# Optimization experiments

Measured on AMD Instinct MI355X. Metric: run time of the kernel, lower is better.

The kernel has to match this reference:

```python
import jax, jax.numpy as jnp
import numpy as np

N, H, C, A, G, NG = 400000, 256, 128, 32, 512, 1024
BN_EPS = 1e-5


def setup_inputs() -> dict:
    key = jax.random.key(0)
    ks = jax.random.split(key, 14)
    s = lambda fan: 1.0 / np.sqrt(fan)
    return {
        "initial_node_states": jax.random.normal(ks[0], (N, H), jnp.float32),
        "final_node_states": jax.random.normal(ks[1], (N, H), jnp.float32),
        "aux_variables": jax.random.normal(ks[2], (NG, A), jnp.float32),
        "graph_nodes_list": jnp.sort(jax.random.randint(ks[3], (N,), 0, NG, jnp.int32)),
        "num_graphs": NG,
        "Wg": jax.random.normal(ks[4], (2 * H, C), jnp.float32) * s(2 * H),
        "bg": jnp.zeros((C,), jnp.float32),
        "Wt": jax.random.normal(ks[5], (H, C), jnp.float32) * s(H),
        "bt": jnp.zeros((C,), jnp.float32),
        "gamma": jnp.ones((C + A,), jnp.float32),
        "beta": jnp.zeros((C + A,), jnp.float32),
        "W1": jax.random.normal(ks[6], (C + A, G), jnp.float32) * s(C + A),
        "b1": jnp.zeros((G,), jnp.float32),
        "W2": jax.random.normal(ks[7], (G, C), jnp.float32) * s(G),
        "b2": jnp.zeros((C,), jnp.float32),
    }


def reference(initial_node_states, final_node_states, aux_variables,
              graph_nodes_list, num_graphs,
              Wg, bg, Wt, bt, gamma, beta, W1, b1, W2, b2):
    # Nodewise gated readout (dropout layers are identity in eval mode)
    gate_input = jnp.concatenate([initial_node_states, final_node_states], axis=-1)  # [N, 2H]
    gate = jax.nn.sigmoid(gate_input @ Wg + bg)                                      # [N, C]
    nodewise = gate * (final_node_states @ Wt + bt)                                  # [N, C]
    # Scatter-add into per-graph buckets (index_add_)
    graph_readout = jax.ops.segment_sum(nodewise, graph_nodes_list, num_segments=num_graphs)  # [NG, C]
    ext = jnp.concatenate([graph_readout, aux_variables], axis=1)                    # [NG, C+A]
    # BatchNorm1d (training-mode batch statistics, biased variance)
    mean = ext.mean(axis=0)
    var = ext.var(axis=0)
    norm = (ext - mean) / jnp.sqrt(var + BN_EPS) * gamma + beta
    # Small MLP head
    hidden = jax.nn.relu(norm @ W1 + b1)
    logits = hidden @ W2 + b2                                                        # [NG, C]
    return logits
```

## Files before the change

kernel.cpp:

```cpp
#include <hip/hip_runtime.h>
#include <hip/hip_bf16.h>

#define NNODES 400000
#define BM 64

typedef __attribute__((ext_vector_type(8))) short  short8;
typedef __attribute__((ext_vector_type(4))) float  floatx4;

typedef unsigned short u16;
typedef unsigned int   u32;

__device__ __forceinline__ short f2bf(float f) {
    u32 u = __builtin_bit_cast(u32, f);
    u += 0x7fffu + ((u >> 16) & 1u);
    return (short)(u >> 16);
}

__device__ __forceinline__ void async16(const void* g, void* l) {
    __builtin_amdgcn_global_load_lds(
        (const __attribute__((address_space(1))) u32*)g,
        (__attribute__((address_space(3))) u32*)l, 16, 0, 0);
}

__global__ __launch_bounds__(256) void k0_build(
    const float* __restrict__ Wg, const float* __restrict__ Wt,
    u16* __restrict__ Bp)
{
    int base = (blockIdx.x * 256 + threadIdx.x) * 4;
    #pragma unroll
    for (int e = 0; e < 4; e++) {
        int idx  = base + e;
        int j    = idx & 7;
        int col  = (idx >> 3) & 255;
        int quad = (idx >> 11) & 3;
        int kc   = idx >> 13;
        int k    = kc * 32 + quad * 8 + j;
        float v;
        if (col < 128)       v = Wg[k * 128 + col];
        else if (k >= 256)   v = Wt[(k - 256) * 128 + (col - 128)];
        else                 v = 0.0f;
        Bp[idx] = (u16)f2bf(v);
    }
}

__global__ __launch_bounds__(256) void k1_gemm(
    const float* __restrict__ initS, const float* __restrict__ finS,
    const int* __restrict__ gids, const u16* __restrict__ Bp,
    const float* __restrict__ bg, const float* __restrict__ bt,
    float* __restrict__ readout)
{
    __shared__ __align__(16) u16  Bl[4][256][8];
    __shared__ float nodew[BM][128];
    __shared__ int   gidL[BM];

    const int tid  = threadIdx.x;
    const int w    = tid >> 6;
    const int lane = tid & 63;
    const int quad = lane >> 4;
    const int l15  = lane & 15;
    const int nodeBase = blockIdx.x * BM;

    if (tid < BM) gidL[tid] = gids[nodeBase + tid];

    floatx4 acc[16];
    #pragma unroll
    for (int i = 0; i < 16; i++) acc[i] = (floatx4){0.f, 0.f, 0.f, 0.f};

    const int rowNode = nodeBase + w * 16 + l15;
    const float* initRow = initS + (size_t)rowNode * 256;
    const float* finRow  = finS  + (size_t)rowNode * 256;
    const int chunk = w * 4;

    for (int kc = 0; kc < 16; kc++) {
        #pragma unroll
        for (int i = 0; i < 4; i++) {
            const u16* gsrc = Bp + (size_t)kc * 8192 + (chunk + i) * 512 + lane * 8;
            u16* ldst = &Bl[0][0][0] + (chunk + i) * 512;
            async16(gsrc, ldst);
        }
        const float* ar = (kc < 8) ? (initRow + kc * 32 + quad * 8)
                                   : (finRow + (kc - 8) * 32 + quad * 8);
        float4 a0 = *reinterpret_cast<const float4*>(ar);
        float4 a1 = *reinterpret_cast<const float4*>(ar + 4);
        short8 af;
        af[0] = f2bf(a0.x); af[1] = f2bf(a0.y); af[2] = f2bf(a0.z); af[3] = f2bf(a0.w);
        af[4] = f2bf(a1.x); af[5] = f2bf(a1.y); af[6] = f2bf(a1.z); af[7] = f2bf(a1.w);

        __syncthreads();
        #pragma unroll
        for (int ct = 0; ct < 16; ct++) {
            short8 bf = *reinterpret_cast<const short8*>(&Bl[quad][ct * 16 + l15][0]);
            acc[ct] = __builtin_amdgcn_mfma_f32_16x16x32_bf16(af, bf, acc[ct], 0, 0, 0);
        }
        __syncthreads();
    }

    #pragma unroll
    for (int ct = 0; ct < 8; ct++) {
        const int c = ct * 16 + l15;
        const float bgv = bg[c];
        const float btv = bt[c];
        #pragma unroll
        for (int i = 0; i < 4; i++) {
            const int r = quad * 4 + i;
            float g = acc[ct][i] + bgv;
            float t = acc[ct + 8][i] + btv;
            float s = 1.0f / (1.0f + __expf(-g));
            nodew[w * 16 + r][c] = s * t;
        }
    }
    __syncthreads();

    {
        const int c  = tid & 127;
        const int r0 = (tid >> 7) * 32;
        float s = 0.f;
        int cur = gidL[r0];
        for (int r = r0; r < r0 + 32; r++) {
            int g = gidL[r];
            if (g != cur) {
                atomicAdd(&readout[cur * 128 + c], s);
                s = 0.f; cur = g;
            }
            s += nodew[r][c];
        }
        atomicAdd(&readout[cur * 128 + c], s);
    }
}

__global__ __launch_bounds__(256) void k2_stats(
    const float* __restrict__ readout, const float* __restrict__ aux,
    const float* __restrict__ gamma, const float* __restrict__ beta,
    float* __restrict__ scale, float* __restrict__ shift)
{
    const int col = blockIdx.x;
    const int tid = threadIdx.x;
    float s = 0.f, q = 0.f;
    for (int g = tid; g < 1024; g += 256) {
        float v = (col < 128) ? readout[g * 128 + col] : aux[g * 32 + (col - 128)];
        s += v; q += v * v;
    }
    #pragma unroll
    for (int off = 32; off > 0; off >>= 1) {
        s += __shfl_down(s, off);
        q += __shfl_down(q, off);
    }
    __shared__ float ps[4], pq[4];
    if ((tid & 63) == 0) { ps[tid >> 6] = s; pq[tid >> 6] = q; }
    __syncthreads();
    if (tid == 0) {
        float S = ps[0] + ps[1] + ps[2] + ps[3];
        float Q = pq[0] + pq[1] + pq[2] + pq[3];
        float mean = S * (1.0f / 1024.0f);
        float var  = Q * (1.0f / 1024.0f) - mean * mean;
        float rstd = rsqrtf(var + 1e-5f);
        float sc   = gamma[col] * rstd;
        scale[col] = sc;
        shift[col] = beta[col] - mean * sc;
    }
}

__global__ __launch_bounds__(256) void k3a_hidden(
    const float* __restrict__ readout, const float* __restrict__ aux,
    const float* __restrict__ scale, const float* __restrict__ shift,
    const float* __restrict__ W1, const float* __restrict__ b1,
    float* __restrict__ hidden)
{
    const int g0  = blockIdx.x * 4;
    const int tid = threadIdx.x;
    const float* r0 = readout + (size_t)g0 * 128;
    const float* a0 = aux     + (size_t)g0 * 32;

    #pragma unroll
    for (int jj = 0; jj < 2; jj++) {
        const int j = tid + jj * 256;
        float acc0 = 0.f, acc1 = 0.f, acc2 = 0.f, acc3 = 0.f, accS = 0.f;
        for (int k = 0; k < 128; k++) {
            float wv = W1[k * 512 + j];
            accS += shift[k] * wv;
            float wsv = scale[k] * wv;
            acc0 += r0[k]       * wsv;
            acc1 += r0[128 + k] * wsv;
            acc2 += r0[256 + k] * wsv;
            acc3 += r0[384 + k] * wsv;
        }
        for (int k = 0; k < 32; k++) {
            float wv = W1[(128 + k) * 512 + j];
            accS += shift[128 + k] * wv;
            float wsv = scale[128 + k] * wv;
            acc0 += a0[k]      * wsv;
            acc1 += a0[32 + k] * wsv;
            acc2 += a0[64 + k] * wsv;
            acc3 += a0[96 + k] * wsv;
        }
        float bb = b1[j] + accS;
        hidden[(size_t)(g0 + 0) * 512 + j] = fmaxf(acc0 + bb, 0.f);
        hidden[(size_t)(g0 + 1) * 512 + j] = fmaxf(acc1 + bb, 0.f);
        hidden[(size_t)(g0 + 2) * 512 + j] = fmaxf(acc2 + bb, 0.f);
        hidden[(size_t)(g0 + 3) * 512 + j] = fmaxf(acc3 + bb, 0.f);
    }
}

__global__ __launch_bounds__(256) void k3b_logits(
    const float* __restrict__ hidden, const float* __restrict__ W2,
    const float* __restrict__ b2, float* __restrict__ out)
{
    const int g0  = blockIdx.x * 4;
    const int tid = threadIdx.x;
    const int j   = tid & 127;
    const int rh  = tid >> 7;
    const float* h0 = hidden + (size_t)(g0 + rh * 2) * 512;
    float acc0 = 0.f, acc1 = 0.f;
    for (int k = 0; k < 512; k++) {
        float wv = W2[k * 128 + j];
        acc0 += h0[k]       * wv;
        acc1 += h0[512 + k] * wv;
    }
    float bb = b2[j];
    out[(size_t)(g0 + rh * 2 + 0) * 128 + j] = acc0 + bb;
    out[(size_t)(g0 + rh * 2 + 1) * 128 + j] = acc1 + bb;
}

extern "C" void kernel_launch(void* const* d_in, const int* in_sizes, int n_in,
                              void* d_out, int out_size, void* d_ws, size_t ws_size,
                              hipStream_t stream)
{
    const float* initS = (const float*)d_in[0];
    const float* finS  = (const float*)d_in[1];
    const float* aux   = (const float*)d_in[2];
    const int*   gid   = (const int*)d_in[3];
    const float* Wg    = (const float*)d_in[5];
    const float* bg    = (const float*)d_in[6];
    const float* Wt    = (const float*)d_in[7];
    const float* bt    = (const float*)d_in[8];
    const float* gamma = (const float*)d_in[9];
    const float* beta  = (const float*)d_in[10];
    const float* W1    = (const float*)d_in[11];
    const float* b1    = (const float*)d_in[12];
    const float* W2    = (const float*)d_in[13];
    const float* b2    = (const float*)d_in[14];
    float* out = (float*)d_out;

    char* ws = (char*)d_ws;
    u16*   Bp      = (u16*)(ws + 0);
    float* readout = (float*)(ws + 262144);
    float* scale   = (float*)(ws + 786432);
    float* shift   = (float*)(ws + 787456);
    float* hidden  = (float*)(ws + 1048576);

    k0_build  <<<128, 256, 0, stream>>>(Wg, Wt, Bp);
    hipMemsetAsync(readout, 0, 1024 * 128 * sizeof(float), stream);
    k1_gemm   <<<NNODES / BM, 256, 0, stream>>>(initS, finS, gid, Bp, bg, bt, readout);
    k2_stats  <<<160, 256, 0, stream>>>(readout, aux, gamma, beta, scale, shift);
    k3a_hidden<<<256, 256, 0, stream>>>(readout, aux, scale, shift, W1, b1, hidden);
    k3b_logits<<<256, 256, 0, stream>>>(hidden, W2, b2, out);
}
```

Before: 935.5 us.

## Double-buffer weight tiles, skip zero Wt block, and reduce segments in registers

```diff
diff --git a/kernel.cpp b/kernel.cpp
--- a/kernel.cpp
+++ b/kernel.cpp
@@ -29,29 +29,31 @@
     int base = (blockIdx.x * 256 + threadIdx.x) * 4;
     #pragma unroll
     for (int e = 0; e < 4; e++) {
-        int idx  = base + e;
-        int j    = idx & 7;
-        int col  = (idx >> 3) & 255;
-        int quad = (idx >> 11) & 3;
-        int kc   = idx >> 13;
-        int k    = kc * 32 + quad * 8 + j;
+        int idx   = base + e;
+        int local = idx & 4095;
+        int quad  = local >> 10;
+        int col   = (local >> 3) & 127;
+        int j     = local & 7;
         float v;
-        if (col < 128)       v = Wg[k * 128 + col];
-        else if (k >= 256)   v = Wt[(k - 256) * 128 + (col - 128)];
-        else                 v = 0.0f;
+        if (idx < 65536) {
+            int kc = idx >> 12;
+            v = Wg[(kc * 32 + quad * 8 + j) * 128 + col];
+        } else {
+            int kct = (idx - 65536) >> 12;
+            v = Wt[(kct * 32 + quad * 8 + j) * 128 + col];
+        }
         Bp[idx] = (u16)f2bf(v);
     }
 }
 
-__global__ __launch_bounds__(256) void k1_gemm(
+__global__ __launch_bounds__(256, 4) void k1_gemm(
     const float* __restrict__ initS, const float* __restrict__ finS,
     const int* __restrict__ gids, const u16* __restrict__ Bp,
     const float* __restrict__ bg, const float* __restrict__ bt,
     float* __restrict__ readout)
 {
-    __shared__ __align__(16) u16  Bl[4][256][8];
-    __shared__ float nodew[BM][128];
-    __shared__ int   gidL[BM];
+    __shared__ __align__(16) u16 Bl[2][8192];
+    __shared__ int gidL[BM];
 
     const int tid  = threadIdx.x;
     const int w    = tid >> 6;
@@ -62,69 +64,123 @@
 
     if (tid < BM) gidL[tid] = gids[nodeBase + tid];
 
-    floatx4 acc[16];
+    floatx4 accg[8], acct[8];
     #pragma unroll
-    for (int i = 0; i < 16; i++) acc[i] = (floatx4){0.f, 0.f, 0.f, 0.f};
+    for (int i = 0; i < 8; i++) {
+        accg[i] = (floatx4){0.f, 0.f, 0.f, 0.f};
+        acct[i] = (floatx4){0.f, 0.f, 0.f, 0.f};
+    }
 
     const int rowNode = nodeBase + w * 16 + l15;
     const float* initRow = initS + (size_t)rowNode * 256;
     const float* finRow  = finS  + (size_t)rowNode * 256;
-    const int chunk = w * 4;
+
+    auto stage = [&](int kc, u16* lbuf) {
+        if (kc < 8) {
+            #pragma unroll
+            for (int i = 0; i < 2; i++) {
+                int c = w * 2 + i;
+                async16(Bp + (size_t)kc * 4096 + c * 512 + lane * 8, lbuf + c * 512);
+            }
+        } else {
+            #pragma unroll
+            for (int i = 0; i < 4; i++) {
+                int c = w * 4 + i;
+                const u16* src = (c < 8)
+                    ? (Bp + (size_t)kc * 4096 + c * 512)
+                    : (Bp + 65536 + (size_t)(kc - 8) * 4096 + (c - 8) * 512);
+                async16(src + lane * 8, lbuf + c * 512);
+            }
+        }
+    };
+
+    stage(0, Bl[0]);
+    const float* ar = initRow + quad * 8;
+    float4 a0 = *reinterpret_cast<const float4*>(ar);
+    float4 a1 = *reinterpret_cast<const float4*>(ar + 4);
 
     for (int kc = 0; kc < 16; kc++) {
-        #pragma unroll
-        for (int i = 0; i < 4; i++) {
-            const u16* gsrc = Bp + (size_t)kc * 8192 + (chunk + i) * 512 + lane * 8;
-            u16* ldst = &Bl[0][0][0] + (chunk + i) * 512;
-            async16(gsrc, ldst);
-        }
-        const float* ar = (kc < 8) ? (initRow + kc * 32 + quad * 8)
-                                   : (finRow + (kc - 8) * 32 + quad * 8);
-        float4 a0 = *reinterpret_cast<const float4*>(ar);
-        float4 a1 = *reinterpret_cast<const float4*>(ar + 4);
+        const u16* cur = Bl[kc & 1];
+        __syncthreads();
+
+        float4 a0n, a1n;
+        if (kc < 15) {
+            stage(kc + 1, Bl[(kc + 1) & 1]);
+            const float* arn = ((kc + 1) < 8)
+                ? (initRow + (kc + 1) * 32 + quad * 8)
+                : (finRow + (kc + 1 - 8) * 32 + quad * 8);
+            a0n = *reinterpret_cast<const float4*>(arn);
+            a1n = *reinterpret_cast<const float4*>(arn + 4);
+        }
+
         short8 af;
         af[0] = f2bf(a0.x); af[1] = f2bf(a0.y); af[2] = f2bf(a0.z); af[3] = f2bf(a0.w);
         af[4] = f2bf(a1.x); af[5] = f2bf(a1.y); af[6] = f2bf(a1.z); af[7] = f2bf(a1.w);
 
-        __syncthreads();
-        #pragma unroll
-        for (int ct = 0; ct < 16; ct++) {
-            short8 bf = *reinterpret_cast<const short8*>(&Bl[quad][ct * 16 + l15][0]);
-            acc[ct] = __builtin_amdgcn_mfma_f32_16x16x32_bf16(af, bf, acc[ct], 0, 0, 0);
-        }
-        __syncthreads();
-    }
-
-    #pragma unroll
-    for (int ct = 0; ct < 8; ct++) {
-        const int c = ct * 16 + l15;
-        const float bgv = bg[c];
-        const float btv = bt[c];
+        #pragma unroll
+        for (int ct = 0; ct < 8; ct++) {
+            short8 bf = *reinterpret_cast<const short8*>(
+                cur + quad * 1024 + (ct * 16 + l15) * 8);
+            accg[ct] = __builtin_amdgcn_mfma_f32_16x16x32_bf16(af, bf, accg[ct], 0, 0, 0);
+        }
+        if (kc >= 8) {
+            #pragma unroll
+            for (int ct = 0; ct < 8; ct++) {
+                short8 bf = *reinterpret_cast<const short8*>(
+                    cur + 4096 + quad * 1024 + (ct * 16 + l15) * 8);
+                acct[ct] = __builtin_amdgcn_mfma_f32_16x16x32_bf16(af, bf, acct[ct], 0, 0, 0);
+            }
+        }
+        a0 = a0n; a1 = a1n;
+    }
+
+    const int rbase = w * 16;
+    const int gFirst = gidL[rbase];
+    const int gLast  = gidL[rbase + 15];
+
+    if (gFirst == gLast) {
+        #pragma unroll
+        for (int ct = 0; ct < 8; ct++) {
+            const float bgv = bg[ct * 16 + l15];
+            const float btv = bt[ct * 16 + l15];
+            float s = 0.f;
+            #pragma unroll
+            for (int i = 0; i < 4; i++) {
+                float g = accg[ct][i] + bgv;
+                float t = acct[ct][i] + btv;
+                s += t / (1.0f + __expf(-g));
+            }
+            s += __shfl_xor(s, 16);
+            s += __shfl_xor(s, 32);
+            if ((ct >> 1) == quad)
+                atomicAdd(&readout[gFirst * 128 + ct * 16 + l15], s);
+        }
+    } else {
+        float s[8];
+        #pragma unroll
+        for (int ct = 0; ct < 8; ct++) s[ct] = 0.f;
+        int curg = gidL[rbase + quad * 4];
         #pragma unroll
         for (int i = 0; i < 4; i++) {
-            const int r = quad * 4 + i;
-            float g = acc[ct][i] + bgv;
-            float t = acc[ct + 8][i] + btv;
-            float s = 1.0f / (1.0f + __expf(-g));
-            nodew[w * 16 + r][c] = s * t;
-        }
-    }
-    __syncthreads();
-
-    {
-        const int c  = tid & 127;
-        const int r0 = (tid >> 7) * 32;
-        float s = 0.f;
-        int cur = gidL[r0];
-        for (int r = r0; r < r0 + 32; r++) {
-            int g = gidL[r];
-            if (g != cur) {
-                atomicAdd(&readout[cur * 128 + c], s);
-                s = 0.f; cur = g;
-            }
-            s += nodew[r][c];
-        }
-        atomicAdd(&readout[cur * 128 + c], s);
+            int g = gidL[rbase + quad * 4 + i];
+            if (g != curg) {
+                #pragma unroll
+                for (int ct = 0; ct < 8; ct++) {
+                    atomicAdd(&readout[curg * 128 + ct * 16 + l15], s[ct]);
+                    s[ct] = 0.f;
+                }
+                curg = g;
+            }
+            #pragma unroll
+            for (int ct = 0; ct < 8; ct++) {
+                float gg = accg[ct][i] + bg[ct * 16 + l15];
+                float tt = acct[ct][i] + bt[ct * 16 + l15];
+                s[ct] += tt / (1.0f + __expf(-gg));
+            }
+        }
+        #pragma unroll
+        for (int ct = 0; ct < 8; ct++)
+            atomicAdd(&readout[curg * 128 + ct * 16 + l15], s[ct]);
     }
 }
 
@@ -248,7 +304,7 @@
     float* shift   = (float*)(ws + 787456);
     float* hidden  = (float*)(ws + 1048576);
 
-    k0_build  <<<128, 256, 0, stream>>>(Wg, Wt, Bp);
+    k0_build  <<<96, 256, 0, stream>>>(Wg, Wt, Bp);
     hipMemsetAsync(readout, 0, 1024 * 128 * sizeof(float), stream);
     k1_gemm   <<<NNODES / BM, 256, 0, stream>>>(initS, finS, gid, Bp, bg, bt, readout);
     k2_stats  <<<160, 256, 0, stream>>>(readout, aux, gamma, beta, scale, shift);
```

Result: no change. 925.3 us (-1.1%).
